# Performance work log

Hardware: AMD Instinct MI355X
Metric: run time of the kernel (lower is better)

The kernel has to match this reference:

```python
import jax, jax.numpy as jnp
import numpy as np

TEMP = 0.07
EPS = 1e-8
NUM_CLASSES = 7
THRESH = 0.3


def setup_inputs() -> dict:
    key = jax.random.key(0)
    k1, k2, k3, k4, k5 = jax.random.split(key, 5)
    N, H, E, C = 8192, 128, 256, NUM_CLASSES
    reps = jax.random.normal(k1, (N, H), dtype=jnp.float32)
    labels = jax.random.randint(k2, (N,), 0, C, dtype=jnp.int64 if jax.config.jax_enable_x64 else jnp.int32)
    centers = jax.random.normal(k3, (C, E), dtype=jnp.float32)
    fc_w = jax.random.normal(k4, (H, E), dtype=jnp.float32) * (1.0 / np.sqrt(E))
    fc_b = jax.random.normal(k5, (H,), dtype=jnp.float32) * 0.01
    return {"reps": reps, "labels": labels, "centers": centers, "fc_w": fc_w, "fc_b": fc_b}


def reference(reps, labels, centers, fc_w, fc_b):
    # fc(default_centers): [C, H]
    curr_centers = centers @ fc_w.T + fc_b
    pad_labels = jnp.arange(NUM_CLASSES, dtype=labels.dtype)

    all_reps = jnp.concatenate([reps, curr_centers], axis=0)      # [M, H]
    all_labels = jnp.concatenate([labels, pad_labels], axis=0)    # [M]
    B = reps.shape[0]
    M = all_reps.shape[0]

    # cosine similarity via normalized matmul (avoids [B,M,H] broadcast)
    norms = jnp.sqrt(jnp.sum(all_reps * all_reps, axis=-1))
    rn = all_reps / jnp.maximum(norms, 1e-8)[:, None]
    cos = rn[:B] @ rn.T                                           # [B, M]

    scores = (1.0 + cos) * 0.5 + EPS
    eye = (jnp.arange(B)[:, None] == jnp.arange(M)[None, :]).astype(scores.dtype)
    scores = scores * (1.0 - eye) / TEMP
    # torch uses .item() on the max -> a non-differentiable constant
    scores = scores - jax.lax.stop_gradient(jnp.max(scores))
    e = jnp.exp(scores)

    pos_mask = (labels[:, None] == all_labels[None, :]).astype(scores.dtype)  # [B, M]
    mask = 1.0 - eye

    pos_sum = jnp.sum(e * pos_mask * mask, axis=-1)
    neg_sum = jnp.sum(e * (1.0 - pos_mask), axis=-1)
    probs = pos_sum / (pos_sum + neg_sum)
    probs = probs / (jnp.sum(pos_mask * mask, axis=-1) + EPS)

    loss_vec = -jnp.log(probs + EPS)
    loss_mask = (loss_vec > THRESH).astype(loss_vec.dtype)
    denom = jax.lax.stop_gradient(jnp.sum(loss_mask)) + EPS
    loss = jnp.sum(loss_vec * loss_mask) / denom
    return loss
```

## Files before the change

### kernel.cpp

```cpp
#include <hip/hip_runtime.h>
#include <hip/hip_bf16.h>

#define BN 8192
#define MM 8199
#define MP 8208
#define HH 128
#define EE 256
#define NTILE 513
#define JCH 32

typedef __attribute__((ext_vector_type(8))) short short8;
typedef __attribute__((ext_vector_type(4))) float floatx4;

__global__ __launch_bounds__(64)
void centers_kernel(const float* __restrict__ centers,
                    const float* __restrict__ fc_w,
                    const float* __restrict__ fc_b,
                    float* __restrict__ curr) {
  int o = blockIdx.x;
  int c = o >> 7, h = o & 127;
  int lane = threadIdx.x;
  const float4* ce = (const float4*)(centers + c * EE);
  const float4* w  = (const float4*)(fc_w + h * EE);
  float4 a = ce[lane];
  float4 b = w[lane];
  float s = a.x * b.x + a.y * b.y + a.z * b.z + a.w * b.w;
#pragma unroll
  for (int m = 1; m < 64; m <<= 1) s += __shfl_xor(s, m);
  if (lane == 0) curr[o] = s + fc_b[h];
}

__global__ __launch_bounds__(64)
void norm_kernel(const float* __restrict__ reps,
                 const float* __restrict__ curr,
                 const int* __restrict__ labels,
                 __hip_bfloat16* __restrict__ rn,
                 int* __restrict__ labp) {
  int r = blockIdx.x;
  int lane = threadIdx.x;
  float2 v = make_float2(0.f, 0.f);
  if (r < BN)      v = ((const float2*)(reps + (size_t)r * HH))[lane];
  else if (r < MM) v = ((const float2*)(curr + (size_t)(r - BN) * HH))[lane];
  float ss = v.x * v.x + v.y * v.y;
#pragma unroll
  for (int m = 1; m < 64; m <<= 1) ss += __shfl_xor(ss, m);
  float inv = 1.0f / fmaxf(sqrtf(ss), 1e-8f);
  __hip_bfloat162 h2;
  h2.x = __float2bfloat16(v.x * inv);
  h2.y = __float2bfloat16(v.y * inv);
  ((__hip_bfloat162*)(rn + (size_t)r * HH))[lane] = h2;
  if (lane == 0) labp[r] = (r < BN) ? labels[r] : (r < MM ? r - BN : -1);
}

__global__ __launch_bounds__(64)
void main_kernel(const __hip_bfloat16* __restrict__ rn,
                 const int* __restrict__ labp,
                 float* __restrict__ tot,
                 float* __restrict__ pos) {
  const int lane = threadIdx.x;
  const int q = lane >> 4, col = lane & 15;
  const int ibase = blockIdx.x * 64;
  const short* rns = (const short*)rn;

  short8 afrag[4][4];
#pragma unroll
  for (int it = 0; it < 4; ++it) {
    const short8* p = (const short8*)(rns + (size_t)(ibase + it * 16 + col) * HH + q * 8);
    afrag[it][0] = p[0];
    afrag[it][1] = p[4];
    afrag[it][2] = p[8];
    afrag[it][3] = p[12];
  }
  int labi[4][4];
#pragma unroll
  for (int it = 0; it < 4; ++it)
#pragma unroll
    for (int r = 0; r < 4; ++r)
      labi[it][r] = labp[ibase + it * 16 + q * 4 + r];

  float stot[4][4] = {};
  float spos[4][4] = {};
  const float K2 = 10.30496147f;

  for (int t = blockIdx.y; t < NTILE; t += JCH) {
    const int jb = t * 16;
    const int jg = jb + col;
    const short8* bp = (const short8*)(rns + (size_t)jg * HH + q * 8);
    short8 b0 = bp[0], b1 = bp[4], b2 = bp[8], b3 = bp[12];
    const int labj = labp[jg];
    const float jvf = (jg < MM) ? 1.f : 0.f;
#pragma unroll
    for (int it = 0; it < 4; ++it) {
      floatx4 acc = {0.f, 0.f, 0.f, 0.f};
      acc = __builtin_amdgcn_mfma_f32_16x16x32_bf16(afrag[it][0], b0, acc, 0, 0, 0);
      acc = __builtin_amdgcn_mfma_f32_16x16x32_bf16(afrag[it][1], b1, acc, 0, 0, 0);
      acc = __builtin_amdgcn_mfma_f32_16x16x32_bf16(afrag[it][2], b2, acc, 0, 0, 0);
      acc = __builtin_amdgcn_mfma_f32_16x16x32_bf16(afrag[it][3], b3, acc, 0, 0, 0);
      const bool isdiag = (jb == ibase + it * 16);
#pragma unroll
      for (int r = 0; r < 4; ++r) {
        float e = exp2f(fmaf(acc[r], K2, -K2)) * jvf;
        if (isdiag && (col == q * 4 + r)) e = 0.f;
        stot[it][r] += e;
        spos[it][r] += (labj == labi[it][r]) ? e : 0.f;
      }
    }
  }

#pragma unroll
  for (int it = 0; it < 4; ++it)
#pragma unroll
    for (int r = 0; r < 4; ++r) {
      float tt = stot[it][r], pp = spos[it][r];
#pragma unroll
      for (int m = 1; m <= 8; m <<= 1) {
        tt += __shfl_xor(tt, m);
        pp += __shfl_xor(pp, m);
      }
      if (col == 0) {
        int i = ibase + it * 16 + q * 4 + r;
        atomicAdd(&tot[i], tt);
        atomicAdd(&pos[i], pp);
      }
    }
}

__global__ __launch_bounds__(256)
void loss_kernel(const float* __restrict__ tot,
                 const float* __restrict__ pos,
                 const int* __restrict__ labels,
                 float* __restrict__ out) {
  __shared__ int hist[8];
  __shared__ float s1[256], s2[256];
  int tid = threadIdx.x;
  if (tid < 8) hist[tid] = 0;
  __syncthreads();
  for (int i = tid; i < BN; i += 256) atomicAdd(&hist[labels[i]], 1);
  __syncthreads();
  float lsum = 0.f, msum = 0.f;
  for (int i = tid; i < BN; i += 256) {
    float t = tot[i], p = pos[i];
    float c = (float)hist[labels[i]];
    float pr = (p / t) / (c + 1e-8f);
    float lv = -logf(pr + 1e-8f);
    if (lv > 0.3f) { lsum += lv; msum += 1.f; }
  }
  s1[tid] = lsum; s2[tid] = msum;
  __syncthreads();
  for (int st = 128; st > 0; st >>= 1) {
    if (tid < st) { s1[tid] += s1[tid + st]; s2[tid] += s2[tid + st]; }
    __syncthreads();
  }
  if (tid == 0) out[0] = s1[0] / (s2[0] + 1e-8f);
}

extern "C" void kernel_launch(void* const* d_in, const int* in_sizes, int n_in,
                              void* d_out, int out_size, void* d_ws, size_t ws_size,
                              hipStream_t stream) {
  const float* reps    = (const float*)d_in[0];
  const int*   labels  = (const int*)d_in[1];
  const float* centers = (const float*)d_in[2];
  const float* fc_w    = (const float*)d_in[3];
  const float* fc_b    = (const float*)d_in[4];
  float* out = (float*)d_out;

  char* ws = (char*)d_ws;
  float* curr = (float*)ws;
  int* labp   = (int*)(ws + 4096);
  __hip_bfloat16* rn = (__hip_bfloat16*)(ws + 40960);
  float* tot = (float*)(ws + 40960 + 2101248);
  float* pos = tot + BN;

  hipMemsetAsync(tot, 0, 2 * BN * sizeof(float), stream);
  centers_kernel<<<896, 64, 0, stream>>>(centers, fc_w, fc_b, curr);
  norm_kernel<<<MP, 64, 0, stream>>>(reps, curr, labels, rn, labp);
  main_kernel<<<dim3(128, JCH), 64, 0, stream>>>(rn, labp, tot, pos);
  loss_kernel<<<1, 256, 0, stream>>>(tot, pos, labels, out);
}
```

Measured before the change: 143.5 us.

## Fuse centers projection into norm kernel, prefetch B tiles, drop pad masking

Merges the center projection into the normalization kernel, which removes one launch, and packs four rows per 256-thread block. The main kernel now runs four waves per block with 32 rows each and software-prefetches the next column tile's fragments and labels. It drops the per-element padding mask and uses the raw exp2 intrinsic. The loss kernel compensates by subtracting the constant contribution of the 9 zero-padded columns. The loss kernel itself widens to 1024 threads. Together these reduce launch count and per-element ALU work and hide load latency, at the cost of halving A-fragment reuse per wave.

```diff
diff --git a/kernel.cpp b/kernel.cpp
--- a/kernel.cpp
+++ b/kernel.cpp
@@ -8,39 +8,42 @@
 #define EE 256
 #define NTILE 513
 #define JCH 32
+#define K2 10.30496147f
 
 typedef __attribute__((ext_vector_type(8))) short short8;
 typedef __attribute__((ext_vector_type(4))) float floatx4;
 
-__global__ __launch_bounds__(64)
-void centers_kernel(const float* __restrict__ centers,
-                    const float* __restrict__ fc_w,
-                    const float* __restrict__ fc_b,
-                    float* __restrict__ curr) {
-  int o = blockIdx.x;
-  int c = o >> 7, h = o & 127;
-  int lane = threadIdx.x;
-  const float4* ce = (const float4*)(centers + c * EE);
-  const float4* w  = (const float4*)(fc_w + h * EE);
-  float4 a = ce[lane];
-  float4 b = w[lane];
-  float s = a.x * b.x + a.y * b.y + a.z * b.z + a.w * b.w;
-#pragma unroll
-  for (int m = 1; m < 64; m <<= 1) s += __shfl_xor(s, m);
-  if (lane == 0) curr[o] = s + fc_b[h];
-}
-
-__global__ __launch_bounds__(64)
+__global__ __launch_bounds__(256)
 void norm_kernel(const float* __restrict__ reps,
-                 const float* __restrict__ curr,
+                 const float* __restrict__ centers,
+                 const float* __restrict__ fc_w,
+                 const float* __restrict__ fc_b,
                  const int* __restrict__ labels,
                  __hip_bfloat16* __restrict__ rn,
                  int* __restrict__ labp) {
-  int r = blockIdx.x;
-  int lane = threadIdx.x;
+  const int lane = threadIdx.x & 63;
+  const int r = blockIdx.x * 4 + (threadIdx.x >> 6);
   float2 v = make_float2(0.f, 0.f);
-  if (r < BN)      v = ((const float2*)(reps + (size_t)r * HH))[lane];
-  else if (r < MM) v = ((const float2*)(curr + (size_t)(r - BN) * HH))[lane];
+  if (r < BN) {
+    v = ((const float2*)(reps + (size_t)r * HH))[lane];
+  } else if (r < MM) {
+    int c = r - BN;
+    const float4* ce = (const float4*)(centers + c * EE);
+    const float4* w0 = (const float4*)(fc_w + (size_t)(2 * lane) * EE);
+    const float4* w1 = (const float4*)(fc_w + (size_t)(2 * lane + 1) * EE);
+    float s0 = 0.f, s1 = 0.f;
+#pragma unroll 8
+    for (int e = 0; e < 64; ++e) {
+      float4 a = ce[e];
+      float4 x = w0[e];
+      float4 y = w1[e];
+      s0 += a.x * x.x + a.y * x.y + a.z * x.z + a.w * x.w;
+      s1 += a.x * y.x + a.y * y.y + a.z * y.z + a.w * y.w;
+    }
+    float2 bb = ((const float2*)fc_b)[lane];
+    v.x = s0 + bb.x;
+    v.y = s1 + bb.y;
+  }
   float ss = v.x * v.x + v.y * v.y;
 #pragma unroll
   for (int m = 1; m < 64; m <<= 1) ss += __shfl_xor(ss, m);
@@ -52,45 +55,52 @@
   if (lane == 0) labp[r] = (r < BN) ? labels[r] : (r < MM ? r - BN : -1);
 }
 
-__global__ __launch_bounds__(64)
+__global__ __launch_bounds__(256, 4)
 void main_kernel(const __hip_bfloat16* __restrict__ rn,
                  const int* __restrict__ labp,
                  float* __restrict__ tot,
                  float* __restrict__ pos) {
-  const int lane = threadIdx.x;
+  const int tid = threadIdx.x;
+  const int lane = tid & 63;
+  const int wv = tid >> 6;
   const int q = lane >> 4, col = lane & 15;
-  const int ibase = blockIdx.x * 64;
+  const int ibase = blockIdx.x * 128 + wv * 32;
   const short* rns = (const short*)rn;
 
-  short8 afrag[4][4];
+  short8 afrag[2][4];
 #pragma unroll
-  for (int it = 0; it < 4; ++it) {
+  for (int it = 0; it < 2; ++it) {
     const short8* p = (const short8*)(rns + (size_t)(ibase + it * 16 + col) * HH + q * 8);
     afrag[it][0] = p[0];
     afrag[it][1] = p[4];
     afrag[it][2] = p[8];
     afrag[it][3] = p[12];
   }
-  int labi[4][4];
+  int labi[2][4];
 #pragma unroll
-  for (int it = 0; it < 4; ++it)
+  for (int it = 0; it < 2; ++it)
 #pragma unroll
     for (int r = 0; r < 4; ++r)
       labi[it][r] = labp[ibase + it * 16 + q * 4 + r];
 
-  float stot[4][4] = {};
-  float spos[4][4] = {};
-  const float K2 = 10.30496147f;
+  float stot[2][4] = {};
+  float spos[2][4] = {};
 
-  for (int t = blockIdx.y; t < NTILE; t += JCH) {
+  int t = blockIdx.y;
+  const short8* bp = (const short8*)(rns + (size_t)(t * 16 + col) * HH + q * 8);
+  short8 b0 = bp[0], b1 = bp[4], b2 = bp[8], b3 = bp[12];
+  int labj = labp[t * 16 + col];
+
+  while (t < NTILE) {
+    const int tn = t + JCH;
+    const int ts = (tn < NTILE) ? tn : t;
+    const short8* np = (const short8*)(rns + (size_t)(ts * 16 + col) * HH + q * 8);
+    short8 n0 = np[0], n1 = np[4], n2 = np[8], n3 = np[12];
+    int labn = labp[ts * 16 + col];
+
     const int jb = t * 16;
-    const int jg = jb + col;
-    const short8* bp = (const short8*)(rns + (size_t)jg * HH + q * 8);
-    short8 b0 = bp[0], b1 = bp[4], b2 = bp[8], b3 = bp[12];
-    const int labj = labp[jg];
-    const float jvf = (jg < MM) ? 1.f : 0.f;
 #pragma unroll
-    for (int it = 0; it < 4; ++it) {
+    for (int it = 0; it < 2; ++it) {
       floatx4 acc = {0.f, 0.f, 0.f, 0.f};
       acc = __builtin_amdgcn_mfma_f32_16x16x32_bf16(afrag[it][0], b0, acc, 0, 0, 0);
       acc = __builtin_amdgcn_mfma_f32_16x16x32_bf16(afrag[it][1], b1, acc, 0, 0, 0);
@@ -99,16 +109,18 @@
       const bool isdiag = (jb == ibase + it * 16);
 #pragma unroll
       for (int r = 0; r < 4; ++r) {
-        float e = exp2f(fmaf(acc[r], K2, -K2)) * jvf;
+        float e = __builtin_amdgcn_exp2f(__builtin_fmaf(acc[r], K2, -K2));
         if (isdiag && (col == q * 4 + r)) e = 0.f;
         stot[it][r] += e;
         spos[it][r] += (labj == labi[it][r]) ? e : 0.f;
       }
     }
+    b0 = n0; b1 = n1; b2 = n2; b3 = n3; labj = labn;
+    t = tn;
   }
 
 #pragma unroll
-  for (int it = 0; it < 4; ++it)
+  for (int it = 0; it < 2; ++it)
 #pragma unroll
     for (int r = 0; r < 4; ++r) {
       float tt = stot[it][r], pp = spos[it][r];
@@ -125,21 +137,22 @@
     }
 }
 
-__global__ __launch_bounds__(256)
+__global__ __launch_bounds__(1024)
 void loss_kernel(const float* __restrict__ tot,
                  const float* __restrict__ pos,
                  const int* __restrict__ labels,
                  float* __restrict__ out) {
   __shared__ int hist[8];
-  __shared__ float s1[256], s2[256];
-  int tid = threadIdx.x;
+  __shared__ float s1[1024], s2[1024];
+  const int tid = threadIdx.x;
   if (tid < 8) hist[tid] = 0;
   __syncthreads();
-  for (int i = tid; i < BN; i += 256) atomicAdd(&hist[labels[i]], 1);
+  for (int i = tid; i < BN; i += 1024) atomicAdd(&hist[labels[i]], 1);
   __syncthreads();
+  const float padc = 9.0f * exp2f(-K2);
   float lsum = 0.f, msum = 0.f;
-  for (int i = tid; i < BN; i += 256) {
-    float t = tot[i], p = pos[i];
+  for (int i = tid; i < BN; i += 1024) {
+    float t = tot[i] - padc, p = pos[i];
     float c = (float)hist[labels[i]];
     float pr = (p / t) / (c + 1e-8f);
     float lv = -logf(pr + 1e-8f);
@@ -147,7 +160,7 @@
   }
   s1[tid] = lsum; s2[tid] = msum;
   __syncthreads();
-  for (int st = 128; st > 0; st >>= 1) {
+  for (int st = 512; st > 0; st >>= 1) {
     if (tid < st) { s1[tid] += s1[tid + st]; s2[tid] += s2[tid + st]; }
     __syncthreads();
   }
@@ -165,15 +178,13 @@
   float* out = (float*)d_out;
 
   char* ws = (char*)d_ws;
-  float* curr = (float*)ws;
-  int* labp   = (int*)(ws + 4096);
+  int* labp = (int*)ws;
   __hip_bfloat16* rn = (__hip_bfloat16*)(ws + 40960);
   float* tot = (float*)(ws + 40960 + 2101248);
   float* pos = tot + BN;
 
   hipMemsetAsync(tot, 0, 2 * BN * sizeof(float), stream);
-  centers_kernel<<<896, 64, 0, stream>>>(centers, fc_w, fc_b, curr);
-  norm_kernel<<<MP, 64, 0, stream>>>(reps, curr, labels, rn, labp);
-  main_kernel<<<dim3(128, JCH), 64, 0, stream>>>(rn, labp, tot, pos);
-  loss_kernel<<<1, 256, 0, stream>>>(tot, pos, labels, out);
+  norm_kernel<<<MP / 4, 256, 0, stream>>>(reps, centers, fc_w, fc_b, labels, rn, labp);
+  main_kernel<<<dim3(BN / 128, JCH), 256, 0, stream>>>(rn, labp, tot, pos);
+  loss_kernel<<<1, 1024, 0, stream>>>(tot, pos, labels, out);
 }
```

Result: slower. 163.0 us (+13.6%).
